# Optimization experiments

Measured on AMD Instinct MI355X. Metric: run time of the kernel, lower is better.

The kernel has to match this reference:

```python
import jax, jax.numpy as jnp
import numpy as np

B, IN, OUT = 131072, 256, 256
BITWIDTH = 7.0


def setup_inputs() -> dict:
    key = jax.random.key(0)
    k1, k2 = jax.random.split(key)
    # simulated int8 activations (integer-valued float32)
    act_in = jax.random.randint(k1, (B, IN), -127, 128).astype(jnp.float32)
    # UniformWeights: xavier_uniform then weight_quant to the int8 grid
    limit = float(np.sqrt(6.0 / (IN + OUT)))
    w = jax.random.uniform(k2, (OUT, IN), minval=-limit, maxval=limit, dtype=jnp.float32)
    w_range = jnp.max(jnp.abs(w))
    weight_exp = (jnp.ceil(jnp.log2(w_range)) - 7.0).astype(jnp.int32)
    weight = jnp.round(w / w_range * 127.0)  # int8-valued float32 [OUT, IN]
    return {"act_in": act_in, "exp_in": jnp.int32(0), "weight": weight, "weight_exp": weight_exp}


def _round_shift(x, shift):
    # RoundShift: floor-div by 2**shift, add floor(|remainder| / 2**(shift-1)), clip to int8
    two_s = jnp.exp2(shift)
    rt = jnp.floor(x / two_s)
    prob = jnp.abs(x - rt * two_s)
    dec = jnp.floor(prob / jnp.exp2(shift - 1.0))
    return jnp.clip(rt + dec, -127.0, 127.0)


def reference(act_in, exp_in, weight, weight_exp):
    # int8 GEMM simulated in fp32 (exact: |acc| < 2^24)
    temp = act_in @ weight.T  # [B, OUT] int32 accumulator values
    # RangeEstimate: full-tensor abs-max -> bitwidth
    r = jnp.max(jnp.abs(temp))
    bw = jnp.where(r > 0, jnp.ceil(jnp.log2(jnp.maximum(r, 1.0))), 0.0)
    shift = bw - BITWIDTH
    pos = shift > 0
    safe_shift = jnp.maximum(shift, 1.0)
    rounded = _round_shift(temp, safe_shift)
    act_out = jnp.where(pos, rounded, temp).astype(jnp.int8)
    exp_sum = jnp.asarray(exp_in, jnp.int32) + jnp.asarray(weight_exp, jnp.int32)
    exp_out = (exp_sum + jnp.where(pos, shift, 0.0).astype(jnp.int32)).astype(jnp.int16)
    return act_out, exp_out
```

## Files before the change

### kernel.cpp

```cpp
#include <hip/hip_runtime.h>
#include <stdint.h>


#define M_ROWS 131072
#define NK 256
#define BM 128
#define BK 64
#define BKP 72

typedef __attribute__((ext_vector_type(8))) short bf16x8;
typedef __attribute__((ext_vector_type(4))) float f32x4;
typedef __attribute__((ext_vector_type(4))) float fv4;
typedef __attribute__((ext_vector_type(4))) int iv4;
typedef __attribute__((ext_vector_type(4))) unsigned int u32x4;
typedef __attribute__((ext_vector_type(4))) unsigned short us4;

__device__ __forceinline__ uint32_t pack_bf16(float a, float b) {
  return __builtin_amdgcn_perm(__float_as_uint(b), __float_as_uint(a),
                               0x07060302u);
}

__global__ void wconv(const float* __restrict__ w, unsigned short* __restrict__ wb,
                      int* __restrict__ gmax) {
  if (blockIdx.x == 0 && threadIdx.x == 0) *gmax = 0;
  const int i = blockIdx.x * 256 + threadIdx.x;
  const fv4 f = ((const fv4*)w)[i];
  us4 o;
  o.x = (unsigned short)(__float_as_uint(f.x) >> 16);
  o.y = (unsigned short)(__float_as_uint(f.y) >> 16);
  o.z = (unsigned short)(__float_as_uint(f.z) >> 16);
  o.w = (unsigned short)(__float_as_uint(f.w) >> 16);
  ((us4*)wb)[i] = o;
}

__global__ __launch_bounds__(512, 2) void gemm_maxstore(
    const float* __restrict__ act, const unsigned short* __restrict__ wgtb,
    int* __restrict__ out, int* __restrict__ gmax)
{
  __shared__ __align__(16) short As[BM * BKP];
  __shared__ __align__(16) short Bs[NK * BKP];
  __shared__ int smax;
  const int tid = threadIdx.x;
  if (tid == 0) smax = 0;

  const int bm   = blockIdx.x * BM;
  const int lane = tid & 63;
  const int wave = tid >> 6;
  const int wr   = wave >> 2;
  const int wc   = wave & 3;
  const int lm   = lane & 15;
  const int lk   = lane >> 4;

  const int arow = tid >> 3;
  const int aks  = (tid & 7) * 8;
  const int brow = tid >> 3;
  const int bks  = (tid & 7) * 8;

  uint32_t apk[2][4];
  u32x4 breg[4];

#pragma unroll
  for (int j = 0; j < 2; ++j) {
    const float* p = act + (size_t)(bm + arow + j * 64) * NK + aks;
    const fv4 f0 = *(const fv4*)p;
    const fv4 f1 = *((const fv4*)p + 1);
    apk[j][0] = pack_bf16(f0.x, f0.y); apk[j][1] = pack_bf16(f0.z, f0.w);
    apk[j][2] = pack_bf16(f1.x, f1.y); apk[j][3] = pack_bf16(f1.z, f1.w);
  }
#pragma unroll
  for (int j = 0; j < 4; ++j)
    breg[j] = *(const u32x4*)(wgtb + (size_t)(brow + j * 64) * NK + bks);

  f32x4 acc[4][4] = {};

  for (int kt = 0; kt < NK; kt += BK) {
    __syncthreads();
#pragma unroll
    for (int j = 0; j < 2; ++j)
      *(u32x4*)&As[(arow + j * 64) * BKP + aks] = *(const u32x4*)apk[j];
#pragma unroll
    for (int j = 0; j < 4; ++j)
      *(u32x4*)&Bs[(brow + j * 64) * BKP + bks] = breg[j];
    __syncthreads();

    if (kt + BK < NK) {
      const int ktn = kt + BK;
#pragma unroll
      for (int j = 0; j < 2; ++j) {
        const float* p = act + (size_t)(bm + arow + j * 64) * NK + ktn + aks;
        const fv4 f0 = *(const fv4*)p;
        const fv4 f1 = *((const fv4*)p + 1);
        apk[j][0] = pack_bf16(f0.x, f0.y); apk[j][1] = pack_bf16(f0.z, f0.w);
        apk[j][2] = pack_bf16(f1.x, f1.y); apk[j][3] = pack_bf16(f1.z, f1.w);
      }
#pragma unroll
      for (int j = 0; j < 4; ++j)
        breg[j] = *(const u32x4*)(wgtb + (size_t)(brow + j * 64) * NK + ktn + bks);
    }

#pragma unroll
    for (int kk = 0; kk < BK; kk += 32) {
      bf16x8 af[4], bfr[4];
#pragma unroll
      for (int mi = 0; mi < 4; ++mi)
        af[mi] = *(const bf16x8*)&As[(wr * 64 + mi * 16 + lm) * BKP + kk + lk * 8];
#pragma unroll
      for (int ni = 0; ni < 4; ++ni)
        bfr[ni] = *(const bf16x8*)&Bs[(wc * 64 + ni * 16 + lm) * BKP + kk + lk * 8];
#pragma unroll
      for (int mi = 0; mi < 4; ++mi)
#pragma unroll
        for (int ni = 0; ni < 4; ++ni)
          acc[mi][ni] = __builtin_amdgcn_mfma_f32_16x16x32_bf16(
              af[mi], bfr[ni], acc[mi][ni], 0, 0, 0);
    }
  }

  int imax = 0;
#pragma unroll
  for (int mi = 0; mi < 4; ++mi)
#pragma unroll
    for (int ni = 0; ni < 4; ++ni)
#pragma unroll
      for (int r = 0; r < 4; ++r) {
        const int ti = (int)acc[mi][ni][r];
        const int a = ti < 0 ? -ti : ti;
        imax = a > imax ? a : imax;
        const int m = bm + wr * 64 + mi * 16 + lk * 4 + r;
        const int n = wc * 64 + ni * 16 + lm;
        out[(size_t)m * NK + n] = ti;
      }
#pragma unroll
  for (int off = 32; off; off >>= 1) {
    const int o = __shfl_xor(imax, off, 64);
    imax = o > imax ? o : imax;
  }
  if (lane == 0) atomicMax(&smax, imax);
  __syncthreads();
  if (tid == 0) atomicMax(gmax, smax);
}

__global__ __launch_bounds__(256) void quant_pass(
    int* __restrict__ out, const int* __restrict__ gmax,
    const int* __restrict__ exp_in, const int* __restrict__ wexp)
{
  const int rmax = *gmax;
  const int bw = (rmax <= 1) ? 0 : (32 - __clz(rmax - 1));
  const int shift = bw - 7;
  const bool pos = shift > 0;
  const int s = shift < 1 ? 1 : shift;

  const size_t total  = (size_t)M_ROWS * NK / 4;
  const size_t stride = (size_t)gridDim.x * blockDim.x;
  for (size_t i = (size_t)blockIdx.x * blockDim.x + threadIdx.x; i < total;
       i += stride) {
    iv4 t = ((const iv4*)out)[i];
    iv4 q;
#pragma unroll
    for (int j = 0; j < 4; ++j) {
      const int ti = t[j];
      int r;
      if (pos) {
        const int rt = ti >> s;
        const int dec = (ti - (rt << s)) >> (s - 1);
        r = rt + dec;
        r = r > 127 ? 127 : (r < -127 ? -127 : r);
      } else {
        r = (int)(signed char)(ti & 0xFF);
      }
      q[j] = r;
    }
    __builtin_nontemporal_store(q, &((iv4*)out)[i]);
  }

  if (blockIdx.x == 0 && threadIdx.x == 0) {
    const int e = exp_in[0] + wexp[0] + (pos ? shift : 0);
    out[(size_t)M_ROWS * NK] = (int)(short)e;
  }
}

extern "C" void kernel_launch(void* const* d_in, const int* in_sizes, int n_in,
                              void* d_out, int out_size, void* d_ws, size_t ws_size,
                              hipStream_t stream) {
  const float* act   = (const float*)d_in[0];
  const int* exp_in  = (const int*)d_in[1];
  const float* wgt   = (const float*)d_in[2];
  const int* wexp    = (const int*)d_in[3];
  int* gmax          = (int*)d_ws;
  unsigned short* wb = (unsigned short*)((char*)d_ws + 128);

  wconv<<<dim3(64), dim3(256), 0, stream>>>(wgt, wb, gmax);
  gemm_maxstore<<<dim3(M_ROWS / BM), dim3(512), 0, stream>>>(act, wb, (int*)d_out,
                                                             gmax);
  quant_pass<<<dim3(2048), dim3(256), 0, stream>>>((int*)d_out, gmax, exp_in, wexp);
}
```

Baseline: 285.8 us.

## Keep full weight matrix in LDS and stream activations directly into registers

```diff
diff --git a/kernel.cpp b/kernel.cpp
--- a/kernel.cpp
+++ b/kernel.cpp
@@ -4,9 +4,8 @@
 
 #define M_ROWS 131072
 #define NK 256
-#define BM 128
-#define BK 64
-#define BKP 72
+#define BM 256
+#define BST 264
 
 typedef __attribute__((ext_vector_type(8))) short bf16x8;
 typedef __attribute__((ext_vector_type(4))) float f32x4;
@@ -33,86 +32,53 @@
   ((us4*)wb)[i] = o;
 }
 
-__global__ __launch_bounds__(512, 2) void gemm_maxstore(
+__global__ __launch_bounds__(1024, 4) void gemm_maxstore(
     const float* __restrict__ act, const unsigned short* __restrict__ wgtb,
     int* __restrict__ out, int* __restrict__ gmax)
 {
-  __shared__ __align__(16) short As[BM * BKP];
-  __shared__ __align__(16) short Bs[NK * BKP];
+  __shared__ __align__(16) short Bs[NK * BST];
   __shared__ int smax;
   const int tid = threadIdx.x;
   if (tid == 0) smax = 0;
 
-  const int bm   = blockIdx.x * BM;
+  for (int c = tid; c < NK * NK / 8; c += 1024) {
+    const int col = c >> 5;
+    const int k8  = (c & 31) << 3;
+    *(u32x4*)&Bs[col * BST + k8] = ((const u32x4*)wgtb)[c];
+  }
+  __syncthreads();
+
   const int lane = tid & 63;
   const int wave = tid >> 6;
   const int wr   = wave >> 2;
   const int wc   = wave & 3;
   const int lm   = lane & 15;
   const int lk   = lane >> 4;
+  const int bm   = blockIdx.x * BM;
 
-  const int arow = tid >> 3;
-  const int aks  = (tid & 7) * 8;
-  const int brow = tid >> 3;
-  const int bks  = (tid & 7) * 8;
-
-  uint32_t apk[2][4];
-  u32x4 breg[4];
-
-#pragma unroll
-  for (int j = 0; j < 2; ++j) {
-    const float* p = act + (size_t)(bm + arow + j * 64) * NK + aks;
-    const fv4 f0 = *(const fv4*)p;
-    const fv4 f1 = *((const fv4*)p + 1);
-    apk[j][0] = pack_bf16(f0.x, f0.y); apk[j][1] = pack_bf16(f0.z, f0.w);
-    apk[j][2] = pack_bf16(f1.x, f1.y); apk[j][3] = pack_bf16(f1.z, f1.w);
-  }
-#pragma unroll
-  for (int j = 0; j < 4; ++j)
-    breg[j] = *(const u32x4*)(wgtb + (size_t)(brow + j * 64) * NK + bks);
+  const float* abase = act + (size_t)(bm + wr * 64 + lm) * NK + lk * 8;
 
   f32x4 acc[4][4] = {};
-
-  for (int kt = 0; kt < NK; kt += BK) {
-    __syncthreads();
 #pragma unroll
-    for (int j = 0; j < 2; ++j)
-      *(u32x4*)&As[(arow + j * 64) * BKP + aks] = *(const u32x4*)apk[j];
+  for (int kk = 0; kk < 8; ++kk) {
+    bf16x8 bfr[4];
 #pragma unroll
-    for (int j = 0; j < 4; ++j)
-      *(u32x4*)&Bs[(brow + j * 64) * BKP + bks] = breg[j];
-    __syncthreads();
-
-    if (kt + BK < NK) {
-      const int ktn = kt + BK;
+    for (int ni = 0; ni < 4; ++ni)
+      bfr[ni] = *(const bf16x8*)
+          &Bs[(wc * 64 + ni * 16 + lm) * BST + kk * 32 + lk * 8];
 #pragma unroll
-      for (int j = 0; j < 2; ++j) {
-        const float* p = act + (size_t)(bm + arow + j * 64) * NK + ktn + aks;
-        const fv4 f0 = *(const fv4*)p;
-        const fv4 f1 = *((const fv4*)p + 1);
-        apk[j][0] = pack_bf16(f0.x, f0.y); apk[j][1] = pack_bf16(f0.z, f0.w);
-        apk[j][2] = pack_bf16(f1.x, f1.y); apk[j][3] = pack_bf16(f1.z, f1.w);
-      }
-#pragma unroll
-      for (int j = 0; j < 4; ++j)
-        breg[j] = *(const u32x4*)(wgtb + (size_t)(brow + j * 64) * NK + ktn + bks);
-    }
-
-#pragma unroll
-    for (int kk = 0; kk < BK; kk += 32) {
-      bf16x8 af[4], bfr[4];
-#pragma unroll
-      for (int mi = 0; mi < 4; ++mi)
-        af[mi] = *(const bf16x8*)&As[(wr * 64 + mi * 16 + lm) * BKP + kk + lk * 8];
+    for (int mi = 0; mi < 4; ++mi) {
+      const float* p = abase + (size_t)(mi * 16) * NK + kk * 32;
+      const fv4 f0 = *(const fv4*)p;
+      const fv4 f1 = *((const fv4*)p + 1);
+      u32x4 apk;
+      apk.x = pack_bf16(f0.x, f0.y); apk.y = pack_bf16(f0.z, f0.w);
+      apk.z = pack_bf16(f1.x, f1.y); apk.w = pack_bf16(f1.z, f1.w);
+      const bf16x8 af = __builtin_bit_cast(bf16x8, apk);
 #pragma unroll
       for (int ni = 0; ni < 4; ++ni)
-        bfr[ni] = *(const bf16x8*)&Bs[(wc * 64 + ni * 16 + lm) * BKP + kk + lk * 8];
-#pragma unroll
-      for (int mi = 0; mi < 4; ++mi)
-#pragma unroll
-        for (int ni = 0; ni < 4; ++ni)
-          acc[mi][ni] = __builtin_amdgcn_mfma_f32_16x16x32_bf16(
-              af[mi], bfr[ni], acc[mi][ni], 0, 0, 0);
+        acc[mi][ni] = __builtin_amdgcn_mfma_f32_16x16x32_bf16(
+            af, bfr[ni], acc[mi][ni], 0, 0, 0);
     }
   }
 
@@ -190,7 +156,7 @@
   unsigned short* wb = (unsigned short*)((char*)d_ws + 128);
 
   wconv<<<dim3(64), dim3(256), 0, stream>>>(wgt, wb, gmax);
-  gemm_maxstore<<<dim3(M_ROWS / BM), dim3(512), 0, stream>>>(act, wb, (int*)d_out,
-                                                             gmax);
+  gemm_maxstore<<<dim3(M_ROWS / BM), dim3(1024), 0, stream>>>(act, wb, (int*)d_out,
+                                                              gmax);
   quant_pass<<<dim3(2048), dim3(256), 0, stream>>>((int*)d_out, gmax, exp_in, wexp);
 }
```

Result: slower. 293.2 us (+2.6%).
